# Performance work log

Hardware: AMD Instinct MI355X
Metric: run time of the kernel (lower is better)

## Reference

```python
import jax, jax.numpy as jnp
import numpy as np

# static config matching init_kwargs / input_specs
SPATIAL = [(64, 64), (32, 32), (16, 16), (8, 8)]  # (H_l, W_l) per level
LEN = sum(h * w for h, w in SPATIAL)  # 5440
B, C, H, L, P = 4, 256, 8, 4, 4
DH = C // H
DFF = 1024
EPS = 1e-5


def layer_norm(x, g, b):
    m = x.mean(-1, keepdims=True)
    v = ((x - m) ** 2).mean(-1, keepdims=True)
    return (x - m) / jnp.sqrt(v + EPS) * g + b


def msda_core(value, sampling_locations, attn_weights):
    """Multi-scale deformable attention core (bilinear sample + weighted sum).
    value: [B, Len, H, DH]; sampling_locations: [B, Lq, H, L, P, 2] in [0,1];
    attn_weights: [B, Lq, H, L, P]. Returns [B, Lq, C].
    Matches grid_sample(bilinear, align_corners=False, padding_mode='zeros')."""
    Bn, Lq = sampling_locations.shape[0], sampling_locations.shape[1]
    out = jnp.zeros((Bn, H, Lq, DH), value.dtype)
    start = 0
    for l, (Hl, Wl) in enumerate(SPATIAL):
        vl = value[:, start:start + Hl * Wl]          # [B, Hl*Wl, H, DH]
        start += Hl * Wl
        vl = vl.transpose(0, 2, 1, 3)                  # [B, H, Hl*Wl, DH]
        loc = sampling_locations[:, :, :, l].transpose(0, 2, 1, 3, 4)  # [B,H,Lq,P,2]
        # align_corners=False: pixel = loc * size - 0.5
        px = loc[..., 0] * Wl - 0.5
        py = loc[..., 1] * Hl - 0.5
        x0 = jnp.floor(px); y0 = jnp.floor(py)
        wx1 = px - x0; wy1 = py - y0
        x0i = x0.astype(jnp.int32); y0i = y0.astype(jnp.int32)
        samp = jnp.zeros((Bn, H, Lq, P, DH), value.dtype)
        for dx, dy in ((0, 0), (1, 0), (0, 1), (1, 1)):
            ix = x0i + dx; iy = y0i + dy
            w = (wx1 if dx else 1.0 - wx1) * (wy1 if dy else 1.0 - wy1)
            valid = (ix >= 0) & (ix < Wl) & (iy >= 0) & (iy < Hl)
            idx = jnp.clip(iy, 0, Hl - 1) * Wl + jnp.clip(ix, 0, Wl - 1)  # [B,H,Lq,P]
            g = jnp.take_along_axis(vl, idx.reshape(Bn, H, -1)[..., None], axis=2)
            g = g.reshape(Bn, H, Lq, P, DH)
            samp = samp + g * (w * valid)[..., None]
        aw = attn_weights[:, :, :, l].transpose(0, 2, 1, 3)  # [B,H,Lq,P]
        out = out + (samp * aw[..., None]).sum(3)
    return out.transpose(0, 2, 1, 3).reshape(Bn, Lq, C)


def setup_inputs() -> dict:
    key = jax.random.key(0)
    ks = jax.random.split(key, 20)
    inp = {
        'src': jax.random.normal(ks[0], (B, LEN, C), jnp.float32),
        'pos': jax.random.normal(ks[1], (B, LEN, C), jnp.float32),
        'reference_points': jax.random.uniform(ks[2], (B, LEN, L, 2), jnp.float32),
        'spatial_shapes': jnp.array(SPATIAL, dtype=jnp.int32),
        'level_start_index': jnp.array(np.cumsum([0] + [h * w for h, w in SPATIAL[:-1]]), dtype=jnp.int32),
        'valid_ratios': jnp.ones((B, L, 2), jnp.float32),
        # MSDeformAttn params
        'w_off': jax.random.normal(ks[3], (C, H * L * P * 2), jnp.float32) * 0.01,
        'b_off': jax.random.normal(ks[4], (H * L * P * 2,), jnp.float32) * 0.5,
        'w_attn': jax.random.normal(ks[5], (C, H * L * P), jnp.float32) * 0.05,
        'b_attn': jnp.zeros((H * L * P,), jnp.float32),
        'w_val': jax.random.normal(ks[6], (C, C), jnp.float32) * 0.05,
        'b_val': jnp.zeros((C,), jnp.float32),
        'w_out': jax.random.normal(ks[7], (C, C), jnp.float32) * 0.05,
        'b_out': jnp.zeros((C,), jnp.float32),
        # norm1 + FFN + norm2 params
        'g1': jnp.ones((C,), jnp.float32), 'be1': jnp.zeros((C,), jnp.float32),
        'w1': jax.random.normal(ks[8], (C, DFF), jnp.float32) * 0.05,
        'b1': jnp.zeros((DFF,), jnp.float32),
        'w2': jax.random.normal(ks[9], (DFF, C), jnp.float32) * 0.05,
        'b2': jnp.zeros((C,), jnp.float32),
        'g2': jnp.ones((C,), jnp.float32), 'be2': jnp.zeros((C,), jnp.float32),
    }
    return inp


def reference(src, pos, reference_points, spatial_shapes, level_start_index, valid_ratios,
              w_off, b_off, w_attn, b_attn, w_val, b_val, w_out, b_out,
              g1, be1, w1, b1, w2, b2, g2, be2):
    Bn, Lq, _ = src.shape
    q = src + pos  # with_pos_embed
    off = (q @ w_off + b_off).reshape(Bn, Lq, H, L, P, 2)
    aw = jax.nn.softmax((q @ w_attn + b_attn).reshape(Bn, Lq, H, L * P), axis=-1)
    aw = aw.reshape(Bn, Lq, H, L, P)
    # offset normalizer is (W_l, H_l) per level
    norm = jnp.array([[w, h] for h, w in SPATIAL], dtype=src.dtype)  # [L, 2]
    loc = reference_points[:, :, None, :, None, :] + off / norm[None, None, None, :, None, :]
    value = (src @ w_val + b_val).reshape(Bn, Lq, H, DH)  # padding_mask is None
    attn_out = msda_core(value, loc, aw) @ w_out + b_out
    x = layer_norm(src + attn_out, g1, be1)
    ffn = jax.nn.relu(x @ w1 + b1) @ w2 + b2
    return layer_norm(x + ffn, g2, be2)
```

## Files before the change

kernel.cpp:

```cpp
#include <hip/hip_runtime.h>
#include <hip/hip_fp16.h>
#include <math.h>

#define LEN   5440
#define NTOK  21760
#define CDIM  256
#define HEADS 8
#define DFF   1024
#define LEPS  1e-5f

typedef __attribute__((ext_vector_type(8))) _Float16 f16x8;
typedef __attribute__((ext_vector_type(4))) float f32x4;

__device__ __forceinline__ float4 f4_add(float4 a, float4 b) {
    return make_float4(a.x + b.x, a.y + b.y, a.z + b.z, a.w + b.w);
}

__global__ __launch_bounds__(256) void pack_k(const float* __restrict__ w_off,
                                              const float* __restrict__ w_attn,
                                              const float* __restrict__ w_val,
                                              const float* __restrict__ b_off,
                                              const float* __restrict__ b_attn,
                                              const float* __restrict__ b_val,
                                              const float* __restrict__ w_out,
                                              const float* __restrict__ w1,
                                              const float* __restrict__ w2,
                                              __half* __restrict__ WcatT,
                                              __half* __restrict__ woutT,
                                              __half* __restrict__ w1T,
                                              __half* __restrict__ w2T,
                                              float* __restrict__ bcat) {
    const int i = blockIdx.x * 256 + threadIdx.x;
    if (i < 163840) {
        const int c = i >> 8, k = i & 255;
        float v;
        if (c < 256)      v = w_off[k * 256 + c];
        else if (c < 384) v = w_attn[k * 128 + (c - 256)];
        else              v = w_val[k * 256 + (c - 384)];
        WcatT[i] = __float2half(v);
    } else if (i < 229376) {
        const int j = i - 163840, c = j >> 8, k = j & 255;
        woutT[j] = __float2half(w_out[k * 256 + c]);
    } else if (i < 491520) {
        const int j = i - 229376, c = j >> 8, k = j & 255;
        w1T[j] = __float2half(w1[k * 1024 + c]);
    } else if (i < 753664) {
        const int j = i - 491520, c = j >> 10, k = j & 1023;
        w2T[j] = __float2half(w2[k * 256 + c]);
    }
    if (i < 640) {
        bcat[i] = (i < 256) ? b_off[i] : (i < 384) ? b_attn[i - 256] : b_val[i - 384];
    }
}

template <bool AF32, int OMODE>
__global__ __launch_bounds__(256) void hgemm_k(const void* __restrict__ Ap,
                                               const float* __restrict__ A2f,
                                               const __half* __restrict__ Bt,
                                               const float* __restrict__ bias,
                                               float* __restrict__ Cf,
                                               __half* __restrict__ Ch,
                                               int NnF, int NnH, int K, int colSwitch) {
    __shared__ __half As[128][40];
    __shared__ __half Bs[128][40];
    const int bx = blockIdx.x, by = blockIdx.y;
    const int tid = threadIdx.x;
    const int lane = tid & 63;
    const int wave = tid >> 6;
    const int wr = (wave >> 1) * 64;
    const int wc = (wave & 1) * 64;
    const bool useA2 = AF32 && (bx * 128 < colSwitch);

    const __half* Bbase = Bt + (size_t)(bx * 128) * K;

    const int srow = tid >> 1;
    const int sk = (tid & 1) * 16;

    f32x4 acc[4][4];
#pragma unroll
    for (int m = 0; m < 4; ++m)
#pragma unroll
        for (int n = 0; n < 4; ++n) acc[m][n] = (f32x4){0.f, 0.f, 0.f, 0.f};

    const int fr = lane & 15;
    const int fk = (lane >> 4) * 8;

    for (int k0 = 0; k0 < K; k0 += 32) {
        uint4 a0, a1;
        if (AF32) {
            const float* Af = (const float*)Ap + (size_t)(by * 128 + srow) * K + k0 + sk;
            float4 f0 = *(const float4*)(Af + 0);
            float4 f1 = *(const float4*)(Af + 4);
            float4 f2 = *(const float4*)(Af + 8);
            float4 f3 = *(const float4*)(Af + 12);
            if (useA2) {
                const float* Pf = A2f + (size_t)(by * 128 + srow) * K + k0 + sk;
                f0 = f4_add(f0, *(const float4*)(Pf + 0));
                f1 = f4_add(f1, *(const float4*)(Pf + 4));
                f2 = f4_add(f2, *(const float4*)(Pf + 8));
                f3 = f4_add(f3, *(const float4*)(Pf + 12));
            }
            union { __half2 h[8]; uint4 u[2]; } cv;
            cv.h[0] = __floats2half2_rn(f0.x, f0.y);
            cv.h[1] = __floats2half2_rn(f0.z, f0.w);
            cv.h[2] = __floats2half2_rn(f1.x, f1.y);
            cv.h[3] = __floats2half2_rn(f1.z, f1.w);
            cv.h[4] = __floats2half2_rn(f2.x, f2.y);
            cv.h[5] = __floats2half2_rn(f2.z, f2.w);
            cv.h[6] = __floats2half2_rn(f3.x, f3.y);
            cv.h[7] = __floats2half2_rn(f3.z, f3.w);
            a0 = cv.u[0];
            a1 = cv.u[1];
        } else {
            const __half* Ah = (const __half*)Ap + (size_t)(by * 128 + srow) * K + k0 + sk;
            a0 = *(const uint4*)(Ah + 0);
            a1 = *(const uint4*)(Ah + 8);
        }
        const uint4 b0 = *(const uint4*)&Bbase[(size_t)srow * K + k0 + sk];
        const uint4 b1 = *(const uint4*)&Bbase[(size_t)srow * K + k0 + sk + 8];
        __syncthreads();
        *(uint4*)&As[srow][sk]     = a0;
        *(uint4*)&As[srow][sk + 8] = a1;
        *(uint4*)&Bs[srow][sk]     = b0;
        *(uint4*)&Bs[srow][sk + 8] = b1;
        __syncthreads();
        f16x8 af[4], bf[4];
#pragma unroll
        for (int m = 0; m < 4; ++m) af[m] = *(const f16x8*)&As[wr + m * 16 + fr][fk];
#pragma unroll
        for (int n = 0; n < 4; ++n) bf[n] = *(const f16x8*)&Bs[wc + n * 16 + fr][fk];
#pragma unroll
        for (int m = 0; m < 4; ++m)
#pragma unroll
            for (int n = 0; n < 4; ++n)
                acc[m][n] = __builtin_amdgcn_mfma_f32_16x16x32_f16(af[m], bf[n], acc[m][n], 0, 0, 0);
    }

    const int rowb = by * 128 + wr + (lane >> 4) * 4;
    const int colb = bx * 128 + wc + fr;
    float bn[4];
#pragma unroll
    for (int n = 0; n < 4; ++n) bn[n] = bias[colb + n * 16];
    const bool vhalf = (OMODE == 2) || (OMODE == 3 && bx * 128 >= colSwitch);
    const int colh = (OMODE == 3) ? (colb - colSwitch) : colb;
#pragma unroll
    for (int m = 0; m < 4; ++m) {
#pragma unroll
        for (int r = 0; r < 4; ++r) {
            const int row = rowb + m * 16 + r;
#pragma unroll
            for (int n = 0; n < 4; ++n) {
                float v = acc[m][n][r] + bn[n];
                if (OMODE == 2) v = fmaxf(v, 0.f);
                if (vhalf) Ch[(size_t)row * NnH + colh + n * 16] = __float2half(v);
                else       Cf[(size_t)row * NnF + colb + n * 16] = v;
            }
        }
    }
}

__global__ __launch_bounds__(256) void msda_kernel(const float* __restrict__ C1a,
                                                   const __half* __restrict__ Vh,
                                                   const float* __restrict__ refp,
                                                   __half* __restrict__ out) {
    __shared__ int   sIdx[16][17][4];
    __shared__ float sW[16][17][4];
    const int tid = threadIdx.x;
    const int gi = tid >> 4;
    const int si = tid & 15;
    const int n = blockIdx.x * 2 + (gi >> 3);
    const int h = gi & 7;
    const int b = n / LEN;

    {
        const int l = si >> 2, p = si & 3;
        const float lg = C1a[(size_t)n * 384 + 256 + h * 16 + si];
        float mx = lg;
#pragma unroll
        for (int m = 1; m < 16; m <<= 1) mx = fmaxf(mx, __shfl_xor(mx, m, 16));
        const float e = expf(lg - mx);
        float sum = e;
#pragma unroll
        for (int m = 1; m < 16; m <<= 1) sum += __shfl_xor(sum, m, 16);
        const float aw = e / sum;

        const int Wi[4] = {64, 32, 16, 8};
        const int st[4] = {0, 4096, 5120, 5376};
        const int W = Wi[l];
        const float Wf = (float)W;
        const float rx = refp[((size_t)n * 4 + l) * 2 + 0];
        const float ry = refp[((size_t)n * 4 + l) * 2 + 1];
        const float ox = C1a[(size_t)n * 384 + (((h * 4 + l) * 4 + p) * 2 + 0)];
        const float oy = C1a[(size_t)n * 384 + (((h * 4 + l) * 4 + p) * 2 + 1)];
        const float lx = rx + ox / Wf;
        const float ly = ry + oy / Wf;
        const float px = lx * Wf - 0.5f;
        const float py = ly * Wf - 0.5f;
        const float x0f = floorf(px), y0f = floorf(py);
        const float wx1 = px - x0f, wy1 = py - y0f;
        const int x0 = (int)x0f, y0 = (int)y0f;
#pragma unroll
        for (int c = 0; c < 4; ++c) {
            const int dx = c & 1, dy = c >> 1;
            const int ix = x0 + dx, iy = y0 + dy;
            const float wgt = (dx ? wx1 : 1.f - wx1) * (dy ? wy1 : 1.f - wy1);
            const bool valid = (ix >= 0) && (ix < W) && (iy >= 0) && (iy < W);
            const int ixc = min(max(ix, 0), W - 1);
            const int iyc = min(max(iy, 0), W - 1);
            const int pos = st[l] + iyc * W + ixc;
            sIdx[gi][si][c] = ((b * LEN + pos) << 8) + h * 32;
            sW[gi][si][c] = valid ? (aw * wgt) : 0.f;
        }
    }
    __syncthreads();

    float accx = 0.f, accy = 0.f;
    const int ch = si * 2;
#pragma unroll
    for (int s = 0; s < 16; ++s) {
        const int4   idx = *(const int4*)&sIdx[gi][s][0];
        const float4 w   = *(const float4*)&sW[gi][s][0];
        {
            const float2 v = __half22float2(*(const __half2*)&Vh[idx.x + ch]);
            accx = fmaf(w.x, v.x, accx); accy = fmaf(w.x, v.y, accy);
        }
        {
            const float2 v = __half22float2(*(const __half2*)&Vh[idx.y + ch]);
            accx = fmaf(w.y, v.x, accx); accy = fmaf(w.y, v.y, accy);
        }
        {
            const float2 v = __half22float2(*(const __half2*)&Vh[idx.z + ch]);
            accx = fmaf(w.z, v.x, accx); accy = fmaf(w.z, v.y, accy);
        }
        {
            const float2 v = __half22float2(*(const __half2*)&Vh[idx.w + ch]);
            accx = fmaf(w.w, v.x, accx); accy = fmaf(w.w, v.y, accy);
        }
    }
    union { __half2 h2; unsigned u; } O;
    O.h2 = __floats2half2_rn(accx, accy);
    *(unsigned*)&out[(size_t)n * 256 + h * 32 + ch] = O.u;
}

template <bool WH>
__global__ __launch_bounds__(256) void ln_kernel(const float* __restrict__ Y,
                                                 const float* __restrict__ R,
                                                 const float* __restrict__ gm,
                                                 const float* __restrict__ bt,
                                                 float* __restrict__ O,
                                                 __half* __restrict__ OH) {
    const int wave = threadIdx.x >> 6, lane = threadIdx.x & 63;
    const int n = blockIdx.x * 4 + wave;
    const size_t base = (size_t)n * 256 + lane * 4;
    float4 y = *(const float4*)&Y[base];
    float4 r = *(const float4*)&R[base];
    float4 v = f4_add(y, r);
    float s = v.x + v.y + v.z + v.w;
#pragma unroll
    for (int m = 1; m < 64; m <<= 1) s += __shfl_xor(s, m, 64);
    const float mean = s * (1.f / 256.f);
    const float dx = v.x - mean, dy = v.y - mean, dz = v.z - mean, dw = v.w - mean;
    float ss = dx * dx + dy * dy + dz * dz + dw * dw;
#pragma unroll
    for (int m = 1; m < 64; m <<= 1) ss += __shfl_xor(ss, m, 64);
    const float rstd = rsqrtf(ss * (1.f / 256.f) + LEPS);
    const float4 g4 = *(const float4*)&gm[lane * 4];
    const float4 b4 = *(const float4*)&bt[lane * 4];
    float4 o;
    o.x = dx * rstd * g4.x + b4.x;
    o.y = dy * rstd * g4.y + b4.y;
    o.z = dz * rstd * g4.z + b4.z;
    o.w = dw * rstd * g4.w + b4.w;
    *(float4*)&O[base] = o;
    if (WH) {
        union { __half2 h[2]; uint2 u; } Hh;
        Hh.h[0] = __floats2half2_rn(o.x, o.y);
        Hh.h[1] = __floats2half2_rn(o.z, o.w);
        *(uint2*)&OH[base] = Hh.u;
    }
}

extern "C" void kernel_launch(void* const* d_in, const int* in_sizes, int n_in,
                              void* d_out, int out_size, void* d_ws, size_t ws_size,
                              hipStream_t stream) {
    const float* src   = (const float*)d_in[0];
    const float* pos   = (const float*)d_in[1];
    const float* refp  = (const float*)d_in[2];
    const float* w_off  = (const float*)d_in[6];
    const float* b_off  = (const float*)d_in[7];
    const float* w_attn = (const float*)d_in[8];
    const float* b_attn = (const float*)d_in[9];
    const float* w_val  = (const float*)d_in[10];
    const float* b_val  = (const float*)d_in[11];
    const float* w_out  = (const float*)d_in[12];
    const float* b_out  = (const float*)d_in[13];
    const float* g1     = (const float*)d_in[14];
    const float* be1    = (const float*)d_in[15];
    const float* w1     = (const float*)d_in[16];
    const float* b1     = (const float*)d_in[17];
    const float* w2     = (const float*)d_in[18];
    const float* b2     = (const float*)d_in[19];
    const float* g2     = (const float*)d_in[20];
    const float* be2    = (const float*)d_in[21];

    float* ws = (float*)d_ws;
    float*  C1a   = ws + 0;
    __half* Vh    = (__half*)(ws + 8355840);
    __half* msdah = (__half*)(ws + 11141120);
    float*  xbuf  = ws + 13926400;
    __half* xh    = (__half*)(ws + 19496960);
    __half* hh    = (__half*)(ws + 22282240);
    __half* WcatT = (__half*)(ws + 33423360);
    __half* woutT = (__half*)(ws + 33505280);
    __half* w1T   = (__half*)(ws + 33538048);
    __half* w2T   = (__half*)(ws + 33669120);
    float*  bcat  = ws + 33800192;
    float*  ybuf  = C1a;

    pack_k<<<2944, 256, 0, stream>>>(w_off, w_attn, w_val, b_off, b_attn, b_val,
                                     w_out, w1, w2, WcatT, woutT, w1T, w2T, bcat);

    hgemm_k<true, 3><<<dim3(5, 170), 256, 0, stream>>>(
        (const void*)src, pos, WcatT, bcat, C1a, Vh, 384, 256, 256, 384);

    msda_kernel<<<NTOK / 2, 256, 0, stream>>>(C1a, Vh, refp, msdah);

    hgemm_k<false, 0><<<dim3(2, 170), 256, 0, stream>>>(
        (const void*)msdah, nullptr, woutT, b_out, ybuf, nullptr, 256, 256, 256, 0);

    ln_kernel<true><<<NTOK / 4, 256, 0, stream>>>(ybuf, src, g1, be1, xbuf, xh);

    hgemm_k<false, 2><<<dim3(8, 170), 256, 0, stream>>>(
        (const void*)xh, nullptr, w1T, b1, nullptr, hh, 1024, 1024, 256, 0);

    hgemm_k<false, 0><<<dim3(2, 170), 256, 0, stream>>>(
        (const void*)hh, nullptr, w2T, b2, ybuf, nullptr, 256, 256, 1024, 0);

    ln_kernel<false><<<NTOK / 4, 256, 0, stream>>>(ybuf, xbuf, g2, be2, (float*)d_out, nullptr);
}
```

Baseline: 301.2 us.

## Prefetch GEMM tiles into registers, swizzle workgroups, vectorize MSDA gathers

The GEMM kernel now loads the next K-slice of A and B into registers while the current slice is being multiplied, so global loads overlap with MFMA work. It also remaps workgroup IDs in an XCD-aware round-robin order to improve cache locality. The same remap is applied to the MSDA kernel, whose gather now does 16-byte loads of 8 channels per thread across 4 samples, then reduces partial sums with lane shuffles. In exchange, register pressure rises, and the shuffle reduction plus masked stores add instructions.

```diff
diff --git a/kernel.cpp b/kernel.cpp
--- a/kernel.cpp
+++ b/kernel.cpp
@@ -4,8 +4,6 @@
 
 #define LEN   5440
 #define NTOK  21760
-#define CDIM  256
-#define HEADS 8
 #define DFF   1024
 #define LEPS  1e-5f
 
@@ -14,6 +12,12 @@
 
 __device__ __forceinline__ float4 f4_add(float4 a, float4 b) {
     return make_float4(a.x + b.x, a.y + b.y, a.z + b.z, a.w + b.w);
+}
+
+__device__ __forceinline__ int swz8(int lin, int nwg) {
+    const int q = nwg >> 3, r = nwg & 7;
+    const int x = lin & 7, j = lin >> 3;
+    return (x < r ? x * (q + 1) : r * (q + 1) + (x - r) * q) + j;
 }
 
 __global__ __launch_bounds__(256) void pack_k(const float* __restrict__ w_off,
@@ -63,7 +67,11 @@
                                                int NnF, int NnH, int K, int colSwitch) {
     __shared__ __half As[128][40];
     __shared__ __half Bs[128][40];
-    const int bx = blockIdx.x, by = blockIdx.y;
+    const int nbx = gridDim.x;
+    const int nwg = nbx * gridDim.y;
+    const int tile = swz8(blockIdx.y * nbx + blockIdx.x, nwg);
+    const int bx = tile % nbx, by = tile / nbx;
+
     const int tid = threadIdx.x;
     const int lane = tid & 63;
     const int wave = tid >> 6;
@@ -71,11 +79,14 @@
     const int wc = (wave & 1) * 64;
     const bool useA2 = AF32 && (bx * 128 < colSwitch);
 
-    const __half* Bbase = Bt + (size_t)(bx * 128) * K;
-
     const int srow = tid >> 1;
     const int sk = (tid & 1) * 16;
 
+    const __half* Brow   = Bt + (size_t)(bx * 128 + srow) * K + sk;
+    const float*  Afrow  = AF32 ? ((const float*)Ap + (size_t)(by * 128 + srow) * K + sk) : nullptr;
+    const float*  Pfrow  = useA2 ? (A2f + (size_t)(by * 128 + srow) * K + sk) : nullptr;
+    const __half* Ahrow  = AF32 ? nullptr : ((const __half*)Ap + (size_t)(by * 128 + srow) * K + sk);
+
     f32x4 acc[4][4];
 #pragma unroll
     for (int m = 0; m < 4; ++m)
@@ -85,20 +96,36 @@
     const int fr = lane & 15;
     const int fk = (lane >> 4) * 8;
 
+    uint4 a0, a1, b0, b1;
+    float4 ra0, ra1, ra2, ra3, rp0, rp1, rp2, rp3;
+
+    if (AF32) {
+        ra0 = *(const float4*)(Afrow + 0);
+        ra1 = *(const float4*)(Afrow + 4);
+        ra2 = *(const float4*)(Afrow + 8);
+        ra3 = *(const float4*)(Afrow + 12);
+        if (useA2) {
+            rp0 = *(const float4*)(Pfrow + 0);
+            rp1 = *(const float4*)(Pfrow + 4);
+            rp2 = *(const float4*)(Pfrow + 8);
+            rp3 = *(const float4*)(Pfrow + 12);
+        }
+    } else {
+        a0 = *(const uint4*)(Ahrow + 0);
+        a1 = *(const uint4*)(Ahrow + 8);
+    }
+    b0 = *(const uint4*)(Brow + 0);
+    b1 = *(const uint4*)(Brow + 8);
+
     for (int k0 = 0; k0 < K; k0 += 32) {
-        uint4 a0, a1;
+        __syncthreads();
         if (AF32) {
-            const float* Af = (const float*)Ap + (size_t)(by * 128 + srow) * K + k0 + sk;
-            float4 f0 = *(const float4*)(Af + 0);
-            float4 f1 = *(const float4*)(Af + 4);
-            float4 f2 = *(const float4*)(Af + 8);
-            float4 f3 = *(const float4*)(Af + 12);
+            float4 f0 = ra0, f1 = ra1, f2 = ra2, f3 = ra3;
             if (useA2) {
-                const float* Pf = A2f + (size_t)(by * 128 + srow) * K + k0 + sk;
-                f0 = f4_add(f0, *(const float4*)(Pf + 0));
-                f1 = f4_add(f1, *(const float4*)(Pf + 4));
-                f2 = f4_add(f2, *(const float4*)(Pf + 8));
-                f3 = f4_add(f3, *(const float4*)(Pf + 12));
+                f0 = f4_add(f0, rp0);
+                f1 = f4_add(f1, rp1);
+                f2 = f4_add(f2, rp2);
+                f3 = f4_add(f3, rp3);
             }
             union { __half2 h[8]; uint4 u[2]; } cv;
             cv.h[0] = __floats2half2_rn(f0.x, f0.y);
@@ -111,19 +138,34 @@
             cv.h[7] = __floats2half2_rn(f3.z, f3.w);
             a0 = cv.u[0];
             a1 = cv.u[1];
-        } else {
-            const __half* Ah = (const __half*)Ap + (size_t)(by * 128 + srow) * K + k0 + sk;
-            a0 = *(const uint4*)(Ah + 0);
-            a1 = *(const uint4*)(Ah + 8);
-        }
-        const uint4 b0 = *(const uint4*)&Bbase[(size_t)srow * K + k0 + sk];
-        const uint4 b1 = *(const uint4*)&Bbase[(size_t)srow * K + k0 + sk + 8];
-        __syncthreads();
+        }
         *(uint4*)&As[srow][sk]     = a0;
         *(uint4*)&As[srow][sk + 8] = a1;
         *(uint4*)&Bs[srow][sk]     = b0;
         *(uint4*)&Bs[srow][sk + 8] = b1;
         __syncthreads();
+
+        const int kn = k0 + 32;
+        if (kn < K) {
+            if (AF32) {
+                ra0 = *(const float4*)(Afrow + kn + 0);
+                ra1 = *(const float4*)(Afrow + kn + 4);
+                ra2 = *(const float4*)(Afrow + kn + 8);
+                ra3 = *(const float4*)(Afrow + kn + 12);
+                if (useA2) {
+                    rp0 = *(const float4*)(Pfrow + kn + 0);
+                    rp1 = *(const float4*)(Pfrow + kn + 4);
+                    rp2 = *(const float4*)(Pfrow + kn + 8);
+                    rp3 = *(const float4*)(Pfrow + kn + 12);
+                }
+            } else {
+                a0 = *(const uint4*)(Ahrow + kn + 0);
+                a1 = *(const uint4*)(Ahrow + kn + 8);
+            }
+            b0 = *(const uint4*)(Brow + kn + 0);
+            b1 = *(const uint4*)(Brow + kn + 8);
+        }
+
         f16x8 af[4], bf[4];
 #pragma unroll
         for (int m = 0; m < 4; ++m) af[m] = *(const f16x8*)&As[wr + m * 16 + fr][fk];
@@ -163,12 +205,13 @@
                                                    const __half* __restrict__ Vh,
                                                    const float* __restrict__ refp,
                                                    __half* __restrict__ out) {
-    __shared__ int   sIdx[16][17][4];
+    __shared__ int   sOff[16][17][4];
     __shared__ float sW[16][17][4];
     const int tid = threadIdx.x;
     const int gi = tid >> 4;
     const int si = tid & 15;
-    const int n = blockIdx.x * 2 + (gi >> 3);
+    const int tile = swz8(blockIdx.x, gridDim.x);
+    const int n = tile * 2 + (gi >> 3);
     const int h = gi & 7;
     const int b = n / LEN;
 
@@ -208,38 +251,48 @@
             const int ixc = min(max(ix, 0), W - 1);
             const int iyc = min(max(iy, 0), W - 1);
             const int pos = st[l] + iyc * W + ixc;
-            sIdx[gi][si][c] = ((b * LEN + pos) << 8) + h * 32;
+            sOff[gi][si][c] = ((b * LEN + pos) << 9) + (h << 6);
             sW[gi][si][c] = valid ? (aw * wgt) : 0.f;
         }
     }
     __syncthreads();
 
-    float accx = 0.f, accy = 0.f;
-    const int ch = si * 2;
-#pragma unroll
-    for (int s = 0; s < 16; ++s) {
-        const int4   idx = *(const int4*)&sIdx[gi][s][0];
+    const int cbyte = (si & 3) * 16;
+    const int sb = (si >> 2) * 4;
+    float acc[8];
+#pragma unroll
+    for (int j = 0; j < 8; ++j) acc[j] = 0.f;
+    const char* Vb = (const char*)Vh;
+#pragma unroll
+    for (int t = 0; t < 4; ++t) {
+        const int s = sb + t;
+        const int4   off = *(const int4*)&sOff[gi][s][0];
         const float4 w   = *(const float4*)&sW[gi][s][0];
-        {
-            const float2 v = __half22float2(*(const __half2*)&Vh[idx.x + ch]);
-            accx = fmaf(w.x, v.x, accx); accy = fmaf(w.x, v.y, accy);
-        }
-        {
-            const float2 v = __half22float2(*(const __half2*)&Vh[idx.y + ch]);
-            accx = fmaf(w.y, v.x, accx); accy = fmaf(w.y, v.y, accy);
-        }
-        {
-            const float2 v = __half22float2(*(const __half2*)&Vh[idx.z + ch]);
-            accx = fmaf(w.z, v.x, accx); accy = fmaf(w.z, v.y, accy);
-        }
-        {
-            const float2 v = __half22float2(*(const __half2*)&Vh[idx.w + ch]);
-            accx = fmaf(w.w, v.x, accx); accy = fmaf(w.w, v.y, accy);
-        }
-    }
-    union { __half2 h2; unsigned u; } O;
-    O.h2 = __floats2half2_rn(accx, accy);
-    *(unsigned*)&out[(size_t)n * 256 + h * 32 + ch] = O.u;
+        const f16x8 v0 = *(const f16x8*)(Vb + off.x + cbyte);
+        const f16x8 v1 = *(const f16x8*)(Vb + off.y + cbyte);
+        const f16x8 v2 = *(const f16x8*)(Vb + off.z + cbyte);
+        const f16x8 v3 = *(const f16x8*)(Vb + off.w + cbyte);
+#pragma unroll
+        for (int j = 0; j < 8; ++j) {
+            acc[j] = fmaf(w.x, (float)v0[j], acc[j]);
+            acc[j] = fmaf(w.y, (float)v1[j], acc[j]);
+            acc[j] = fmaf(w.z, (float)v2[j], acc[j]);
+            acc[j] = fmaf(w.w, (float)v3[j], acc[j]);
+        }
+    }
+#pragma unroll
+    for (int j = 0; j < 8; ++j) {
+        acc[j] += __shfl_xor(acc[j], 4, 64);
+        acc[j] += __shfl_xor(acc[j], 8, 64);
+    }
+    if (si < 4) {
+        union { __half2 h2[4]; uint4 u; } O;
+        O.h2[0] = __floats2half2_rn(acc[0], acc[1]);
+        O.h2[1] = __floats2half2_rn(acc[2], acc[3]);
+        O.h2[2] = __floats2half2_rn(acc[4], acc[5]);
+        O.h2[3] = __floats2half2_rn(acc[6], acc[7]);
+        *(uint4*)&out[(size_t)n * 256 + h * 32 + si * 8] = O.u;
+    }
 }
 
 template <bool WH>
```

Result: faster. 285.0 us (-5.4%).
